# Kernel tuning notes

Hardware: AMD Instinct MI355X
Metric: run time of the kernel (lower is better)

The kernel has to match this reference:

```python
import jax, jax.numpy as jnp
import numpy as np

B, N, C = 16, 2048, 3           # images, proposals/image, classes (incl. background)
K = 100                         # num_detections kept per class
SCORE_THRESH = 0.05
NMS_THRESH = 0.5
MIN_ANGLE = 10.0                # process_box min width (self.min_angle)
WX, WW = 1.0, 1.0               # box_coder reg_weights
NEG = jnp.float32(-1e9)


def setup_inputs() -> dict:
    key = jax.random.key(0)
    k1, k2, k3, k4 = jax.random.split(key, 4)
    class_logit = jax.random.normal(k1, (B, N, C), jnp.float32)
    box_regression = jax.random.normal(k2, (B, N, 2 * C), jnp.float32) * 0.1
    starts = jax.random.uniform(k3, (B, N), dtype=jnp.float32) * 300.0
    widths = jax.random.uniform(k4, (B, N), dtype=jnp.float32) * 50.0 + 12.0
    proposal = jnp.stack([starts, starts + widths], axis=-1)  # [B,N,2] 1-D intervals
    return {"class_logit": class_logit, "box_regression": box_regression,
            "proposal": proposal, "image_shape": 360}


def _decode(delta, prop):
    w = prop[:, 1] - prop[:, 0]
    ctr = prop[:, 0] + 0.5 * w
    dx = delta[:, 0] / WX
    dw = jnp.minimum(delta[:, 1] / WW, 4.0)  # clamp like torchvision
    pc = dx * w + ctr
    pw = jnp.exp(dw) * w
    return jnp.stack([pc - 0.5 * pw, pc + 0.5 * pw], axis=-1)  # [N,2]


def _iou_1d(a, b):
    inter = jnp.maximum(0.0, jnp.minimum(a[:, None, 1], b[None, :, 1])
                        - jnp.maximum(a[:, None, 0], b[None, :, 0]))
    union = (a[:, None, 1] - a[:, None, 0]) + (b[None, :, 1] - b[None, :, 0]) - inter
    return inter / jnp.maximum(union, 1e-8)  # [Na,Nb]


def _infer_one_class(score, delta, prop, image_shape):
    # score [N], delta [N,2], prop [N,2] -> [K,3] (start, end, score); invalid slots score=NEG
    box = _decode(delta, prop)
    lo = jnp.clip(box[:, 0], 0.0, image_shape)
    hi = jnp.clip(box[:, 1], 0.0, image_shape)
    box = jnp.stack([lo, hi], axis=-1)
    valid = ((hi - lo) >= MIN_ANGLE) & (score >= SCORE_THRESH)
    ms = jnp.where(valid, score, NEG)
    order = jnp.argsort(-ms)
    b = box[order]
    s = ms[order]
    sup = jax.lax.stop_gradient(_iou_1d(b, b)) > NMS_THRESH  # [N,N] bool
    idx = jnp.arange(N)

    def body(keep, i):  # greedy NMS in score order
        kill = sup[i] & keep[i] & (idx > i)
        return keep & ~kill, None

    keep0 = s > 0.5 * NEG
    keep, _ = jax.lax.scan(body, keep0, idx)
    ks = jnp.where(keep, s, NEG)
    top_s, top_i = jax.lax.top_k(ks, K)
    top_b = b[top_i]
    return jnp.concatenate([top_b, top_s[:, None]], axis=-1)  # [K,3]


def reference(class_logit, box_regression, proposal, image_shape):
    img = jnp.float32(image_shape)
    scores = jax.nn.softmax(class_logit, axis=-1)[..., 1:]        # [B,N,C-1] fg classes
    deltas = box_regression.reshape(B, N, C, 2)[:, :, 1:]         # [B,N,C-1,2]
    scores = jnp.moveaxis(scores, -1, 1)                          # [B,C-1,N]
    deltas = jnp.moveaxis(deltas, 2, 1)                           # [B,C-1,N,2]
    f = jax.vmap(jax.vmap(_infer_one_class, in_axes=(0, 0, None, None)),
                 in_axes=(0, 0, 0, None))
    return f(scores, deltas, proposal, img)  # [B, C-1, K, 3]
```

## Files before the change

kernel.cpp:

```cpp
#include <hip/hip_runtime.h>
#include <math.h>

#define B_IMG 16
#define N_PROP 2048
#define C_CLS 3
#define K_OUT 100
#define NTHREADS 1024
#define NWAVES (NTHREADS / 64)
#define NBLK64 (N_PROP / 64)

__device__ __forceinline__ unsigned long long shfl_xor_u64(unsigned long long v, int lx) {
    unsigned int lo = (unsigned int)__shfl_xor((int)(unsigned int)(v & 0xffffffffull), lx, 64);
    unsigned int hi = (unsigned int)__shfl_xor((int)(unsigned int)(v >> 32), lx, 64);
    return ((unsigned long long)hi << 32) | (unsigned long long)lo;
}
__device__ __forceinline__ float readlane_f(float v, int l) {
    return __int_as_float(__builtin_amdgcn_readlane(__float_as_int(v), l));
}
__device__ __forceinline__ bool iou_gt_half(float inter, float uni) {
    double b = (double)fmaxf(uni, 1e-8f);
    return (double)inter * 2.0 > b * 0x1.000001p0;
}

__global__ __launch_bounds__(NTHREADS)
void roiheads_kernel(const float* __restrict__ class_logit,
                     const float* __restrict__ box_reg,
                     const float* __restrict__ proposal,
                     const int* __restrict__ image_shape_p,
                     float* __restrict__ out)
{
#pragma clang fp contract(off)
    __shared__ unsigned long long skey[N_PROP];
    __shared__ float llo[N_PROP], lhi[N_PROP];
    __shared__ float slo[N_PROP], shi[N_PROP];
    __shared__ unsigned char keep[N_PROP];
    __shared__ unsigned short alv[2][N_PROP];
    __shared__ float clo[64], chi[64];
    __shared__ unsigned long long kmask[NBLK64];
    __shared__ int wsum[NWAVES];
    __shared__ int sh_nvalid, sh_ccnt;

    const int tid = threadIdx.x;
    const int lane = tid & 63;
    const int wid = tid >> 6;
    const int img = blockIdx.x >> 1;
    const int cls = blockIdx.x & 1;

    int raw = image_shape_p[0];
    float imgf = (raw > 0 && raw < 1000000) ? (float)raw : __int_as_float(raw);

    if (tid == 0) sh_nvalid = 0;

    const int p0 = (wid << 7) | (lane << 1);
    const int p1 = p0 | 1;

    auto decode = [&](int n) -> unsigned long long {
#pragma clang fp contract(off)
        const float* lg = class_logit + ((size_t)img * N_PROP + n) * C_CLS;
        float l0 = lg[0], l1 = lg[1], l2 = lg[2];
        float mx = fmaxf(l0, fmaxf(l1, l2));
        float e0 = (float)exp((double)(l0 - mx));
        float e1 = (float)exp((double)(l1 - mx));
        float e2 = (float)exp((double)(l2 - mx));
        float denom = (e0 + e1) + e2;
        float ec = (cls == 0) ? e1 : e2;
        float score = ec / denom;

        const float* dr = box_reg + ((size_t)img * N_PROP + n) * (2 * C_CLS) + 2 * (cls + 1);
        float dx = dr[0];
        float dw = fminf(dr[1], 4.0f);
        const float* pp = proposal + ((size_t)img * N_PROP + n) * 2;
        float pA = pp[0], pB = pp[1];
        float w = pB - pA;
        float ctr = pA + 0.5f * w;
        float t = dx * w;
        float pc = t + ctr;
        float pw = (float)exp((double)dw) * w;
        float half = 0.5f * pw;
        float lo = pc - half;
        float hi = pc + half;
        lo = fminf(fmaxf(lo, 0.0f), imgf);
        hi = fminf(fmaxf(hi, 0.0f), imgf);
        bool valid = ((hi - lo) >= 10.0f) && (score >= 0.05f);
        float ms = valid ? score : -1e9f;

        llo[n] = lo; lhi[n] = hi;
        unsigned int u = __float_as_uint(ms);
        unsigned int e = (u & 0x80000000u) ? ~u : (u | 0x80000000u);
        return ((unsigned long long)e << 32) |
               (unsigned long long)(0xFFFFFFFFu - (unsigned int)n);
    };
    unsigned long long r0 = decode(p0);
    unsigned long long r1 = decode(p1);

    auto pass_inreg = [&](int k, int j) {
        if (j == 1) {
            bool desc = ((p0 & k) == 0);
            bool sw = desc ? (r0 < r1) : (r0 > r1);
            if (sw) { unsigned long long t = r0; r0 = r1; r1 = t; }
        } else {
            int lx = j >> 1;
            unsigned long long o0 = shfl_xor_u64(r0, lx);
            unsigned long long o1 = shfl_xor_u64(r1, lx);
            bool desc = ((p0 & k) == 0);
            bool lower = ((p0 & j) == 0);
            bool takeMax = (lower == desc);
            r0 = takeMax ? (r0 > o0 ? r0 : o0) : (r0 < o0 ? r0 : o0);
            r1 = takeMax ? (r1 > o1 ? r1 : o1) : (r1 < o1 ? r1 : o1);
        }
    };

    for (int k = 2; k <= 128; k <<= 1)
        for (int j = k >> 1; j >= 1; j >>= 1)
            pass_inreg(k, j);

    for (int k = 256; k <= N_PROP; k <<= 1) {
        skey[p0] = r0; skey[p1] = r1;
        __syncthreads();
        for (int j = k >> 1; j >= 128; j >>= 1) {
            int i = ((tid & ~(j - 1)) << 1) | (tid & (j - 1));
            int part = i | j;
            unsigned long long a = skey[i], b = skey[part];
            bool desc_blk = ((i & k) == 0);
            bool sw = desc_blk ? (a < b) : (a > b);
            if (sw) { skey[i] = b; skey[part] = a; }
            __syncthreads();
        }
        r0 = skey[p0]; r1 = skey[p1];
        for (int j = 64; j >= 1; j >>= 1)
            pass_inreg(k, j);
    }
    skey[p0] = r0; skey[p1] = r1;
    __syncthreads();

    for (int i = tid; i < N_PROP; i += NTHREADS) {
        unsigned long long kk = skey[i];
        unsigned int e = (unsigned int)(kk >> 32);
        unsigned int sb = (e & 0x80000000u) ? (e & 0x7FFFFFFFu) : ~e;
        float s = __uint_as_float(sb);
        unsigned int n = 0xFFFFFFFFu - (unsigned int)(kk & 0xFFFFFFFFull);
        slo[i] = llo[n];
        shi[i] = lhi[n];
        keep[i] = 0;
        bool v = (s > -5e8f);
        unsigned long long mb = __ballot(v);
        if (lane == 0) atomicAdd(&sh_nvalid, __popcll(mb));
        alv[0][i] = (unsigned short)i;
    }
    __syncthreads();

    int na = sh_nvalid;
    int cur = 0;
    int tk = 0;
    const unsigned long long below = (1ull << lane) - 1ull;

    while (na > 0) {
        const int m = (na < 64) ? na : 64;
        if (tid < 64) {
            bool inr = (lane < m);
            unsigned short p = inr ? alv[cur][lane] : (unsigned short)0;
            float blo = inr ? slo[p] : 0.0f;
            float bhi = inr ? shi[p] : 0.0f;
            float bw = bhi - blo;
            unsigned long long A = (m >= 64) ? ~0ull : ((1ull << m) - 1ull);
            unsigned long long kept = 0;
            while (A) {
                int c = __builtin_ctzll(A);
                float cl = readlane_f(blo, c);
                float ch = readlane_f(bhi, c);
                float inter = fmaxf(fminf(bhi, ch) - fmaxf(blo, cl), 0.0f);
                float uni = bw + (ch - cl) - inter;
                bool kill = (lane > c) && iou_gt_half(inter, uni);
                unsigned long long row = __ballot(kill);
                kept |= (1ull << c);
                A &= ~(row | (1ull << c));
            }
            bool alive = inr && ((kept >> lane) & 1ull);
            if (alive) keep[p] = 1;
            int rank = __popcll(kept & below);
            if (alive) { clo[rank] = blo; chi[rank] = bhi; }
            if (lane == 0) sh_ccnt = __popcll(kept);
        }
        __syncthreads();
        const int cnt = sh_ccnt;
        tk += cnt;
        if (tk >= K_OUT) break;

        float klo = 0.0f, khi = 0.0f;
        if (lane < cnt) { klo = clo[lane]; khi = chi[lane]; }
        int base = 0;
        for (int start = 64; start < na; start += NTHREADS) {
            int t = start + tid;
            unsigned short q = 0;
            bool surv = false;
            if (t < na) {
                q = alv[cur][t];
                float qlo = slo[q], qhi = shi[q];
                float qw = qhi - qlo;
                bool dead = false;
                for (int r = 0; r < cnt; ++r) {
                    float cl = readlane_f(klo, r);
                    float ch = readlane_f(khi, r);
                    float inter = fmaxf(fminf(qhi, ch) - fmaxf(qlo, cl), 0.0f);
                    float uni = qw + (ch - cl) - inter;
                    dead |= iou_gt_half(inter, uni);
                }
                surv = !dead;
            }
            unsigned long long mb = __ballot(surv);
            if (lane == 0) wsum[wid] = __popcll(mb);
            __syncthreads();
            int off = base, tot = base;
            for (int w2 = 0; w2 < NWAVES; ++w2) {
                int c2 = wsum[w2];
                if (w2 < wid) off += c2;
                tot += c2;
            }
            if (surv) alv[cur ^ 1][off + __popcll(mb & below)] = q;
            base = tot;
            __syncthreads();
        }
        na = base;
        cur ^= 1;
    }

    for (int blk = wid; blk < NBLK64; blk += NWAVES) {
        bool kk = keep[blk * 64 + lane] != 0;
        unsigned long long mb = __ballot(kk);
        if (lane == 0) kmask[blk] = mb;
    }
    __syncthreads();
    {
        float* outp = out + (((size_t)img * 2 + cls) * K_OUT) * 3;
        for (int blk = wid; blk < NBLK64; blk += NWAVES) {
            int kc = 0, nc = 0, nk = 0;
            for (int b = 0; b < NBLK64; ++b) {
                int pc = __popcll(kmask[b]);
                nk += pc;
                if (b < blk) { kc += pc; nc += 64 - pc; }
            }
            if (kc >= K_OUT && nk + nc >= K_OUT && nc >= K_OUT) continue;
            int p = blk * 64 + lane;
            unsigned long long mb = kmask[blk];
            bool k = (mb >> lane) & 1ull;
            int rk = kc + __popcll(mb & below);
            int rn = nc + __popcll((~mb) & below);
            if (k) {
                if (rk < K_OUT) {
                    unsigned long long kk2 = skey[p];
                    unsigned int e = (unsigned int)(kk2 >> 32);
                    unsigned int sb = (e & 0x80000000u) ? (e & 0x7FFFFFFFu) : ~e;
                    outp[rk * 3 + 0] = slo[p];
                    outp[rk * 3 + 1] = shi[p];
                    outp[rk * 3 + 2] = __uint_as_float(sb);
                }
            } else {
                int oi = nk + rn;
                if (oi < K_OUT) {
                    outp[oi * 3 + 0] = slo[p];
                    outp[oi * 3 + 1] = shi[p];
                    outp[oi * 3 + 2] = -1e9f;
                }
            }
        }
    }
}

extern "C" void kernel_launch(void* const* d_in, const int* in_sizes, int n_in,
                              void* d_out, int out_size, void* d_ws, size_t ws_size,
                              hipStream_t stream) {
    const float* class_logit = (const float*)d_in[0];
    const float* box_reg     = (const float*)d_in[1];
    const float* prop        = (const float*)d_in[2];
    const int*   image_shape = (const int*)d_in[3];
    float* out = (float*)d_out;

    roiheads_kernel<<<dim3(B_IMG * 2), dim3(NTHREADS), 0, stream>>>(
        class_logit, box_reg, prop, image_shape, out);
}
```

Before: 97.98 us.

## Split decode into a separate wide kernel writing sort keys to workspace

Moves softmax, box decode and key construction out of the 32-block NMS kernel into a separate 128-block kernel. It computes the softmax once per proposal for both foreground classes and stores keys and boxes in workspace. The NMS kernel then loads precomputed keys and gathers boxes from global memory instead of shared memory. This adds a kernel launch and a global memory round trip in exchange for more parallelism in the decode phase.

```diff
diff --git a/kernel.cpp b/kernel.cpp
--- a/kernel.cpp
+++ b/kernel.cpp
@@ -8,6 +8,7 @@
 #define NTHREADS 1024
 #define NWAVES (NTHREADS / 64)
 #define NBLK64 (N_PROP / 64)
+#define NUNITS (B_IMG * N_PROP)
 
 __device__ __forceinline__ unsigned long long shfl_xor_u64(unsigned long long v, int lx) {
     unsigned int lo = (unsigned int)__shfl_xor((int)(unsigned int)(v & 0xffffffffull), lx, 64);
@@ -21,60 +22,46 @@
     double b = (double)fmaxf(uni, 1e-8f);
     return (double)inter * 2.0 > b * 0x1.000001p0;
 }
-
-__global__ __launch_bounds__(NTHREADS)
-void roiheads_kernel(const float* __restrict__ class_logit,
-                     const float* __restrict__ box_reg,
-                     const float* __restrict__ proposal,
-                     const int* __restrict__ image_shape_p,
-                     float* __restrict__ out)
+__device__ __forceinline__ float parse_imgf(int raw) {
+    return (raw > 0 && raw < 1000000) ? (float)raw : __int_as_float(raw);
+}
+
+__global__ __launch_bounds__(256)
+void decode_kernel(const float* __restrict__ class_logit,
+                   const float* __restrict__ box_reg,
+                   const float* __restrict__ proposal,
+                   const int* __restrict__ image_shape_p,
+                   unsigned long long* __restrict__ wskey,
+                   float2* __restrict__ wbox)
 {
 #pragma clang fp contract(off)
-    __shared__ unsigned long long skey[N_PROP];
-    __shared__ float llo[N_PROP], lhi[N_PROP];
-    __shared__ float slo[N_PROP], shi[N_PROP];
-    __shared__ unsigned char keep[N_PROP];
-    __shared__ unsigned short alv[2][N_PROP];
-    __shared__ float clo[64], chi[64];
-    __shared__ unsigned long long kmask[NBLK64];
-    __shared__ int wsum[NWAVES];
-    __shared__ int sh_nvalid, sh_ccnt;
-
-    const int tid = threadIdx.x;
-    const int lane = tid & 63;
-    const int wid = tid >> 6;
-    const int img = blockIdx.x >> 1;
-    const int cls = blockIdx.x & 1;
-
-    int raw = image_shape_p[0];
-    float imgf = (raw > 0 && raw < 1000000) ? (float)raw : __int_as_float(raw);
-
-    if (tid == 0) sh_nvalid = 0;
-
-    const int p0 = (wid << 7) | (lane << 1);
-    const int p1 = p0 | 1;
-
-    auto decode = [&](int n) -> unsigned long long {
-#pragma clang fp contract(off)
-        const float* lg = class_logit + ((size_t)img * N_PROP + n) * C_CLS;
-        float l0 = lg[0], l1 = lg[1], l2 = lg[2];
-        float mx = fmaxf(l0, fmaxf(l1, l2));
-        float e0 = (float)exp((double)(l0 - mx));
-        float e1 = (float)exp((double)(l1 - mx));
-        float e2 = (float)exp((double)(l2 - mx));
-        float denom = (e0 + e1) + e2;
-        float ec = (cls == 0) ? e1 : e2;
-        float score = ec / denom;
-
-        const float* dr = box_reg + ((size_t)img * N_PROP + n) * (2 * C_CLS) + 2 * (cls + 1);
-        float dx = dr[0];
-        float dw = fminf(dr[1], 4.0f);
-        const float* pp = proposal + ((size_t)img * N_PROP + n) * 2;
-        float pA = pp[0], pB = pp[1];
-        float w = pB - pA;
-        float ctr = pA + 0.5f * w;
-        float t = dx * w;
-        float pc = t + ctr;
+    const int t = blockIdx.x * 256 + threadIdx.x;
+    const int n = t & (N_PROP - 1);
+    const float imgf = parse_imgf(image_shape_p[0]);
+
+    const float* lg = class_logit + (size_t)t * C_CLS;
+    float l0 = lg[0], l1 = lg[1], l2 = lg[2];
+    float mx = fmaxf(l0, fmaxf(l1, l2));
+    float e0 = (float)exp((double)(l0 - mx));
+    float e1 = (float)exp((double)(l1 - mx));
+    float e2 = (float)exp((double)(l2 - mx));
+    float denom = (e0 + e1) + e2;
+
+    const float* pp = proposal + (size_t)t * 2;
+    float pA = pp[0], pB = pp[1];
+    float w = pB - pA;
+    float ctr = pA + 0.5f * w;
+
+    const float* dr = box_reg + (size_t)t * (2 * C_CLS);
+    float d1x = dr[2], d1w = dr[3], d2x = dr[4], d2w = dr[5];
+
+#pragma unroll
+    for (int c = 0; c < 2; ++c) {
+        float score = ((c == 0) ? e1 : e2) / denom;
+        float dx = (c == 0) ? d1x : d2x;
+        float dw = fminf((c == 0) ? d1w : d2w, 4.0f);
+        float tt = dx * w;
+        float pc = tt + ctr;
         float pw = (float)exp((double)dw) * w;
         float half = 0.5f * pw;
         float lo = pc - half;
@@ -83,15 +70,43 @@
         hi = fminf(fmaxf(hi, 0.0f), imgf);
         bool valid = ((hi - lo) >= 10.0f) && (score >= 0.05f);
         float ms = valid ? score : -1e9f;
-
-        llo[n] = lo; lhi[n] = hi;
         unsigned int u = __float_as_uint(ms);
         unsigned int e = (u & 0x80000000u) ? ~u : (u | 0x80000000u);
-        return ((unsigned long long)e << 32) |
-               (unsigned long long)(0xFFFFFFFFu - (unsigned int)n);
-    };
-    unsigned long long r0 = decode(p0);
-    unsigned long long r1 = decode(p1);
+        wskey[c * NUNITS + t] = ((unsigned long long)e << 32) |
+                                (unsigned long long)(0xFFFFFFFFu - (unsigned int)n);
+        wbox[c * NUNITS + t] = make_float2(lo, hi);
+    }
+}
+
+__global__ __launch_bounds__(NTHREADS)
+void roiheads_kernel(const unsigned long long* __restrict__ wskey,
+                     const float2* __restrict__ wbox,
+                     float* __restrict__ out)
+{
+#pragma clang fp contract(off)
+    __shared__ unsigned long long skey[N_PROP];
+    __shared__ float slo[N_PROP], shi[N_PROP];
+    __shared__ unsigned char keep[N_PROP];
+    __shared__ unsigned short alv[2][N_PROP];
+    __shared__ float clo[64], chi[64];
+    __shared__ unsigned long long kmask[NBLK64];
+    __shared__ int wsum[NWAVES];
+    __shared__ int sh_nvalid, sh_ccnt;
+
+    const int tid = threadIdx.x;
+    const int lane = tid & 63;
+    const int wid = tid >> 6;
+    const int img = blockIdx.x >> 1;
+    const int cls = blockIdx.x & 1;
+    const size_t base = (size_t)cls * NUNITS + (size_t)img * N_PROP;
+
+    if (tid == 0) sh_nvalid = 0;
+
+    const int p0 = (wid << 7) | (lane << 1);
+    const int p1 = p0 | 1;
+
+    unsigned long long r0 = wskey[base + p0];
+    unsigned long long r1 = wskey[base + p1];
 
     auto pass_inreg = [&](int k, int j) {
         if (j == 1) {
@@ -139,8 +154,9 @@
         unsigned int sb = (e & 0x80000000u) ? (e & 0x7FFFFFFFu) : ~e;
         float s = __uint_as_float(sb);
         unsigned int n = 0xFFFFFFFFu - (unsigned int)(kk & 0xFFFFFFFFull);
-        slo[i] = llo[n];
-        shi[i] = lhi[n];
+        float2 bx = wbox[base + n];
+        slo[i] = bx.x;
+        shi[i] = bx.y;
         keep[i] = 0;
         bool v = (s > -5e8f);
         unsigned long long mb = __ballot(v);
@@ -188,7 +204,7 @@
 
         float klo = 0.0f, khi = 0.0f;
         if (lane < cnt) { klo = clo[lane]; khi = chi[lane]; }
-        int base = 0;
+        int base2 = 0;
         for (int start = 64; start < na; start += NTHREADS) {
             int t = start + tid;
             unsigned short q = 0;
@@ -210,17 +226,17 @@
             unsigned long long mb = __ballot(surv);
             if (lane == 0) wsum[wid] = __popcll(mb);
             __syncthreads();
-            int off = base, tot = base;
+            int off = base2, tot = base2;
             for (int w2 = 0; w2 < NWAVES; ++w2) {
                 int c2 = wsum[w2];
                 if (w2 < wid) off += c2;
                 tot += c2;
             }
             if (surv) alv[cur ^ 1][off + __popcll(mb & below)] = q;
-            base = tot;
+            base2 = tot;
             __syncthreads();
         }
-        na = base;
+        na = base2;
         cur ^= 1;
     }
 
@@ -275,6 +291,11 @@
     const int*   image_shape = (const int*)d_in[3];
     float* out = (float*)d_out;
 
+    unsigned long long* wskey = (unsigned long long*)d_ws;
+    float2* wbox = (float2*)((char*)d_ws + 2 * NUNITS * sizeof(unsigned long long));
+
+    decode_kernel<<<dim3(NUNITS / 256), dim3(256), 0, stream>>>(
+        class_logit, box_reg, prop, image_shape, wskey, wbox);
     roiheads_kernel<<<dim3(B_IMG * 2), dim3(NTHREADS), 0, stream>>>(
-        class_logit, box_reg, prop, image_shape, out);
-}
+        wskey, wbox, out);
+}
```

Result: no change. 99.51 us (+1.6%).
